# Performance work log

Measured on AMD Instinct MI355X. Metric: run time of the kernel, lower is better.

Reference implementation:

```python
import jax, jax.numpy as jnp
import numpy as np

D_MODEL = 1024
BATCH, HEADS, SEQ, D_HEAD = 4, 16, 2048, D_MODEL // 16


def setup_inputs() -> dict:
    key = jax.random.key(0)
    k1, k2, k3, k4 = jax.random.split(key, 4)
    B = jax.random.normal(k1, (BATCH, HEADS, SEQ, SEQ), dtype=jnp.float32)
    v = jax.random.normal(k2, (BATCH, HEADS, SEQ, D_HEAD), dtype=jnp.float32)
    W = jax.random.normal(k3, (D_MODEL, D_MODEL), dtype=jnp.float32) * (1.0 / np.sqrt(D_MODEL))
    b = jax.random.normal(k4, (D_MODEL,), dtype=jnp.float32) * 0.01
    return {"B": B, "v": v, "W": W, "b": b}


def reference(B, v, W, b):
    # softmax over last (key) axis of the synthesized logits
    p = jax.nn.softmax(B, axis=-1)                      # [b, h, s, s]
    attn = jnp.einsum("bhqk,bhkd->bhqd", p, v)          # [b, h, s, d_head]
    # permute(0,2,3,1): [b, s, d_head, h], then flatten to [b, s, d_model]
    attn = jnp.transpose(attn, (0, 2, 3, 1))
    attn = attn.reshape(attn.shape[0], attn.shape[1], -1)
    # nn.Linear: x @ W.T + b
    return attn @ W.T + b
```

## Files before the change

### kernel.cpp

```cpp
#include <hip/hip_runtime.h>
#include <hip/hip_bf16.h>
#include <stdint.h>


typedef __attribute__((ext_vector_type(8))) short short8;
typedef __attribute__((ext_vector_type(4))) float float4v;

#define SEQL 2048
#define DH   64
#define NH   16
#define DM   1024

static __device__ inline unsigned short f2bf(float x) {
    unsigned u = __float_as_uint(x);
    unsigned r = (u + 0x7FFFu + ((u >> 16) & 1u)) >> 16;
    return (unsigned short)r;
}

__global__ __launch_bounds__(256) void wperm_kernel(const float* __restrict__ W,
                                                    unsigned short* __restrict__ Wp) {
    int tid = blockIdx.x * 256 + threadIdx.x;
    int j   = tid >> 10;
    int rem = tid & 1023;
    int h   = rem >> 6;
    int d   = rem & 63;
    Wp[tid] = f2bf(W[j * 1024 + d * 16 + h]);
}

__global__ __launch_bounds__(256) void attn_kernel(const float* __restrict__ B,
                                                   const float* __restrict__ V,
                                                   unsigned short* __restrict__ attn_out) {
    __shared__ __align__(16) unsigned short Pb[64 * 72];
    __shared__ __align__(16) unsigned short Vt[64 * 72];
    __shared__ float den[64];

    const int t     = threadIdx.x;
    const int lane  = t & 63;
    const int wv    = t >> 6;
    const int c     = lane & 15;
    const int quad  = lane >> 4;
    const int qtile = blockIdx.x;
    const int bh    = blockIdx.y;

    const long long Bbase = (long long)bh * SEQL * SEQL + (long long)(qtile * 64) * SEQL;
    const int Vbase = bh * (SEQL * DH);

    const int sq  = t >> 2;
    const int skb = (t & 3) * 16;
    const int vd  = t & 63;
    const int vko = (t >> 6) * 16;

    if ((t & 3) == 0) den[sq] = 0.0f;

    float4v acc[4];
#pragma unroll
    for (int i = 0; i < 4; i++) acc[i] = (float4v){0.f, 0.f, 0.f, 0.f};

    for (int kk = 0; kk < SEQL / 64; ++kk) {
        {
            const float* src = B + Bbase + (long long)sq * SEQL + (kk * 64 + skb);
            float xv[16];
            *(float4*)&xv[0]  = ((const float4*)src)[0];
            *(float4*)&xv[4]  = ((const float4*)src)[1];
            *(float4*)&xv[8]  = ((const float4*)src)[2];
            *(float4*)&xv[12] = ((const float4*)src)[3];
            alignas(16) unsigned short pk[16];
            float s = 0.0f;
#pragma unroll
            for (int j = 0; j < 16; j++) {
                float e = __expf(xv[j]);
                s += e;
                pk[j] = f2bf(e);
            }
            *(uint4*)&Pb[sq * 72 + skb]     = *(uint4*)&pk[0];
            *(uint4*)&Pb[sq * 72 + skb + 8] = *(uint4*)&pk[8];
            s += __shfl_xor(s, 1);
            s += __shfl_xor(s, 2);
            if ((t & 3) == 0) den[sq] += s;
        }
        {
            const float* vsrc = V + Vbase + (kk * 64 + vko) * DH + vd;
            alignas(16) unsigned short vp[16];
#pragma unroll
            for (int j = 0; j < 16; j++) vp[j] = f2bf(vsrc[j * DH]);
            *(uint4*)&Vt[vd * 72 + vko]     = *(uint4*)&vp[0];
            *(uint4*)&Vt[vd * 72 + vko + 8] = *(uint4*)&vp[8];
        }
        __syncthreads();
#pragma unroll
        for (int ks = 0; ks < 2; ks++) {
            short8 a = *(const short8*)&Pb[(wv * 16 + c) * 72 + ks * 32 + quad * 8];
#pragma unroll
            for (int nb = 0; nb < 4; nb++) {
                short8 bf = *(const short8*)&Vt[(nb * 16 + c) * 72 + ks * 32 + quad * 8];
                acc[nb] = __builtin_amdgcn_mfma_f32_16x16x32_bf16(a, bf, acc[nb], 0, 0, 0);
            }
        }
        __syncthreads();
    }

#pragma unroll
    for (int rr = 0; rr < 4; rr++) {
        int ql  = wv * 16 + quad * 4 + rr;
        float inv = 1.0f / den[ql];
        int qg  = qtile * 64 + ql;
        unsigned short* dst = attn_out + bh * (SEQL * DH) + qg * DH;
#pragma unroll
        for (int nb = 0; nb < 4; nb++) {
            int d = nb * 16 + c;
            dst[d] = f2bf(acc[nb][rr] * inv);
        }
    }
}

__global__ __launch_bounds__(256) void gemm_kernel(const unsigned short* __restrict__ X,
                                                   const unsigned short* __restrict__ Wp,
                                                   const float* __restrict__ bias,
                                                   float* __restrict__ out) {
    __shared__ __align__(16) unsigned short As[128 * 72];
    __shared__ __align__(16) unsigned short Bs[128 * 72];

    const int t    = threadIdx.x;
    const int lane = t & 63;
    const int wv   = t >> 6;
    const int wm   = wv & 1;
    const int wn   = wv >> 1;
    const int c    = lane & 15;
    const int quad = lane >> 4;

    const int rbase = blockIdx.x * 128;
    const int cbase = blockIdx.y * 128;
    const int b     = rbase >> 11;
    const int q0    = rbase & 2047;

    const int srow = t >> 1;
    const int sseg = (t & 1) * 32;

    float4v acc[4][4];
#pragma unroll
    for (int i = 0; i < 4; i++)
#pragma unroll
        for (int j = 0; j < 4; j++) acc[i][j] = (float4v){0.f, 0.f, 0.f, 0.f};

    for (int kt = 0; kt < 16; ++kt) {
        const unsigned short* asrc = X + (((b * 16 + kt) * 2048 + q0 + srow) * 64 + sseg);
        const unsigned short* bsrc = Wp + ((cbase + srow) * 1024 + kt * 64 + sseg);
        uint4 a0 = ((const uint4*)asrc)[0];
        uint4 a1 = ((const uint4*)asrc)[1];
        uint4 a2 = ((const uint4*)asrc)[2];
        uint4 a3 = ((const uint4*)asrc)[3];
        uint4 b0 = ((const uint4*)bsrc)[0];
        uint4 b1 = ((const uint4*)bsrc)[1];
        uint4 b2 = ((const uint4*)bsrc)[2];
        uint4 b3 = ((const uint4*)bsrc)[3];
        *(uint4*)&As[srow * 72 + sseg]      = a0;
        *(uint4*)&As[srow * 72 + sseg + 8]  = a1;
        *(uint4*)&As[srow * 72 + sseg + 16] = a2;
        *(uint4*)&As[srow * 72 + sseg + 24] = a3;
        *(uint4*)&Bs[srow * 72 + sseg]      = b0;
        *(uint4*)&Bs[srow * 72 + sseg + 8]  = b1;
        *(uint4*)&Bs[srow * 72 + sseg + 16] = b2;
        *(uint4*)&Bs[srow * 72 + sseg + 24] = b3;
        __syncthreads();
#pragma unroll
        for (int ks = 0; ks < 2; ks++) {
            short8 af[4], bfr[4];
#pragma unroll
            for (int i = 0; i < 4; i++)
                af[i] = *(const short8*)&As[(wm * 64 + i * 16 + c) * 72 + ks * 32 + quad * 8];
#pragma unroll
            for (int j = 0; j < 4; j++)
                bfr[j] = *(const short8*)&Bs[(wn * 64 + j * 16 + c) * 72 + ks * 32 + quad * 8];
#pragma unroll
            for (int i = 0; i < 4; i++)
#pragma unroll
                for (int j = 0; j < 4; j++)
                    acc[i][j] = __builtin_amdgcn_mfma_f32_16x16x32_bf16(af[i], bfr[j], acc[i][j], 0, 0, 0);
        }
        __syncthreads();
    }

#pragma unroll
    for (int i = 0; i < 4; i++) {
#pragma unroll
        for (int rr = 0; rr < 4; rr++) {
            int row = rbase + wm * 64 + i * 16 + quad * 4 + rr;
            float* orow = out + (long long)row * 1024 + cbase + wn * 64;
            const float* brow = bias + cbase + wn * 64;
#pragma unroll
            for (int j = 0; j < 4; j++) {
                int col = j * 16 + c;
                orow[col] = acc[i][j][rr] + brow[col];
            }
        }
    }
}

extern "C" void kernel_launch(void* const* d_in, const int* in_sizes, int n_in,
                              void* d_out, int out_size, void* d_ws, size_t ws_size,
                              hipStream_t stream) {
    const float* B    = (const float*)d_in[0];
    const float* V    = (const float*)d_in[1];
    const float* W    = (const float*)d_in[2];
    const float* bias = (const float*)d_in[3];
    float* out        = (float*)d_out;

    unsigned short* attn = (unsigned short*)d_ws;
    unsigned short* Wp   = attn + 4 * NH * SEQL * DH;

    wperm_kernel<<<dim3(4096), dim3(256), 0, stream>>>(W, Wp);
    attn_kernel<<<dim3(32, 64), dim3(256), 0, stream>>>(B, V, attn);
    gemm_kernel<<<dim3(64, 8), dim3(256), 0, stream>>>(attn, Wp, bias, out);
}
```

Baseline: 1.423 ms.

## Pre-transpose V to bf16 and stream softmax logits directly into MFMA registers

Adds a kernel that converts V to bf16 and transposes it into a [bh, d, seq] workspace. The attention kernel then has each wave load its B-logit fragments and Vt fragments straight from global memory into MFMA operand registers. This removes the shared-memory staging, both __syncthreads per tile, and the strided per-element V loads. Exp and packing use the hardware v_cvt_pk_bf16_f32 instruction, and the row sum is reduced with shuffles. The cost is an extra launch and an extra pass over V, and each block re-reads Vt from global/L2 instead of sharing it through LDS.

After: 1.537 ms. +8.0%, slower.

```diff
diff --git a/kernel.cpp b/kernel.cpp
--- a/kernel.cpp
+++ b/kernel.cpp
@@ -1,5 +1,4 @@
 #include <hip/hip_runtime.h>
-#include <hip/hip_bf16.h>
 #include <stdint.h>
 
 
@@ -27,88 +26,99 @@
     Wp[tid] = f2bf(W[j * 1024 + d * 16 + h]);
 }
 
-__global__ __launch_bounds__(256) void attn_kernel(const float* __restrict__ B,
-                                                   const float* __restrict__ V,
-                                                   unsigned short* __restrict__ attn_out) {
-    __shared__ __align__(16) unsigned short Pb[64 * 72];
-    __shared__ __align__(16) unsigned short Vt[64 * 72];
-    __shared__ float den[64];
-
-    const int t     = threadIdx.x;
-    const int lane  = t & 63;
-    const int wv    = t >> 6;
-    const int c     = lane & 15;
-    const int quad  = lane >> 4;
-    const int qtile = blockIdx.x;
-    const int bh    = blockIdx.y;
-
-    const long long Bbase = (long long)bh * SEQL * SEQL + (long long)(qtile * 64) * SEQL;
-    const int Vbase = bh * (SEQL * DH);
-
-    const int sq  = t >> 2;
-    const int skb = (t & 3) * 16;
-    const int vd  = t & 63;
-    const int vko = (t >> 6) * 16;
-
-    if ((t & 3) == 0) den[sq] = 0.0f;
+__global__ __launch_bounds__(256) void vtperm_kernel(const float* __restrict__ V,
+                                                     unsigned short* __restrict__ Vt) {
+    __shared__ __align__(16) unsigned short T[64 * 72];
+    const int t  = threadIdx.x;
+    const int bh = blockIdx.y;
+    const int k0 = blockIdx.x * 64;
+    {
+        const int kl = t >> 2;
+        const int d0 = (t & 3) * 16;
+        const float* src = V + ((long long)(bh * SEQL + k0 + kl)) * DH + d0;
+        float x[16];
+        *(float4*)&x[0]  = ((const float4*)src)[0];
+        *(float4*)&x[4]  = ((const float4*)src)[1];
+        *(float4*)&x[8]  = ((const float4*)src)[2];
+        *(float4*)&x[12] = ((const float4*)src)[3];
+#pragma unroll
+        for (int j = 0; j < 16; j++) T[(d0 + j) * 72 + kl] = f2bf(x[j]);
+    }
+    __syncthreads();
+    {
+        const int dd = t >> 2;
+        const int ks = (t & 3) * 16;
+        unsigned short* dst = Vt + ((long long)(bh * DH + dd)) * SEQL + k0 + ks;
+        *(uint4*)dst       = *(uint4*)&T[dd * 72 + ks];
+        *(uint4*)(dst + 8) = *(uint4*)&T[dd * 72 + ks + 8];
+    }
+}
+
+__global__ __launch_bounds__(256, 2) void attn_kernel(const float* __restrict__ B,
+                                                      const unsigned short* __restrict__ Vt,
+                                                      unsigned short* __restrict__ attn_out) {
+    const int t    = threadIdx.x;
+    const int lane = t & 63;
+    const int wv   = t >> 6;
+    const int c    = lane & 15;
+    const int quad = lane >> 4;
+    const int qt   = blockIdx.x;
+    const int bh   = blockIdx.y;
+    const int q0   = qt * 64 + wv * 16;
+
+    const float* Brow = B + ((long long)(bh * SEQL + q0 + c)) * SEQL + quad * 8;
+    const unsigned short* Vb = Vt + ((long long)(bh * DH + c)) * SEQL + quad * 8;
 
     float4v acc[4];
 #pragma unroll
     for (int i = 0; i < 4; i++) acc[i] = (float4v){0.f, 0.f, 0.f, 0.f};
-
-    for (int kk = 0; kk < SEQL / 64; ++kk) {
-        {
-            const float* src = B + Bbase + (long long)sq * SEQL + (kk * 64 + skb);
-            float xv[16];
-            *(float4*)&xv[0]  = ((const float4*)src)[0];
-            *(float4*)&xv[4]  = ((const float4*)src)[1];
-            *(float4*)&xv[8]  = ((const float4*)src)[2];
-            *(float4*)&xv[12] = ((const float4*)src)[3];
-            alignas(16) unsigned short pk[16];
-            float s = 0.0f;
-#pragma unroll
-            for (int j = 0; j < 16; j++) {
-                float e = __expf(xv[j]);
-                s += e;
-                pk[j] = f2bf(e);
-            }
-            *(uint4*)&Pb[sq * 72 + skb]     = *(uint4*)&pk[0];
-            *(uint4*)&Pb[sq * 72 + skb + 8] = *(uint4*)&pk[8];
-            s += __shfl_xor(s, 1);
-            s += __shfl_xor(s, 2);
-            if ((t & 3) == 0) den[sq] += s;
-        }
-        {
-            const float* vsrc = V + Vbase + (kk * 64 + vko) * DH + vd;
-            alignas(16) unsigned short vp[16];
-#pragma unroll
-            for (int j = 0; j < 16; j++) vp[j] = f2bf(vsrc[j * DH]);
-            *(uint4*)&Vt[vd * 72 + vko]     = *(uint4*)&vp[0];
-            *(uint4*)&Vt[vd * 72 + vko + 8] = *(uint4*)&vp[8];
-        }
-        __syncthreads();
-#pragma unroll
-        for (int ks = 0; ks < 2; ks++) {
-            short8 a = *(const short8*)&Pb[(wv * 16 + c) * 72 + ks * 32 + quad * 8];
-#pragma unroll
-            for (int nb = 0; nb < 4; nb++) {
-                short8 bf = *(const short8*)&Vt[(nb * 16 + c) * 72 + ks * 32 + quad * 8];
-                acc[nb] = __builtin_amdgcn_mfma_f32_16x16x32_bf16(a, bf, acc[nb], 0, 0, 0);
-            }
-        }
-        __syncthreads();
-    }
-
+    float den = 0.f;
+
+    for (int kk = 0; kk < SEQL; kk += 64) {
+        float x[16];
+        *(float4*)&x[0]  = *(const float4*)(Brow + kk);
+        *(float4*)&x[4]  = *(const float4*)(Brow + kk + 4);
+        *(float4*)&x[8]  = *(const float4*)(Brow + kk + 32);
+        *(float4*)&x[12] = *(const float4*)(Brow + kk + 36);
+
+        short8 bfr0[4], bfr1[4];
+#pragma unroll
+        for (int nb = 0; nb < 4; nb++) {
+            bfr0[nb] = *(const short8*)(Vb + nb * 16 * SEQL + kk);
+            bfr1[nb] = *(const short8*)(Vb + nb * 16 * SEQL + kk + 32);
+        }
+
+        float s = 0.f;
+#pragma unroll
+        for (int j = 0; j < 16; j++) { x[j] = __expf(x[j]); s += x[j]; }
+        den += s;
+
+        union { unsigned int u[8]; short8 v[2]; } A;
+#pragma unroll
+        for (int j = 0; j < 8; j++) {
+            unsigned int r;
+            asm("v_cvt_pk_bf16_f32 %0, %1, %2" : "=v"(r) : "v"(x[2 * j]), "v"(x[2 * j + 1]));
+            A.u[j] = r;
+        }
+
+#pragma unroll
+        for (int nb = 0; nb < 4; nb++) {
+            acc[nb] = __builtin_amdgcn_mfma_f32_16x16x32_bf16(A.v[0], bfr0[nb], acc[nb], 0, 0, 0);
+            acc[nb] = __builtin_amdgcn_mfma_f32_16x16x32_bf16(A.v[1], bfr1[nb], acc[nb], 0, 0, 0);
+        }
+    }
+
+    den += __shfl_xor(den, 16);
+    den += __shfl_xor(den, 32);
+
+    unsigned short* dst0 = attn_out + ((long long)(bh * SEQL + q0)) * DH;
 #pragma unroll
     for (int rr = 0; rr < 4; rr++) {
-        int ql  = wv * 16 + quad * 4 + rr;
-        float inv = 1.0f / den[ql];
-        int qg  = qtile * 64 + ql;
-        unsigned short* dst = attn_out + bh * (SEQL * DH) + qg * DH;
+        const int ql = quad * 4 + rr;
+        const float inv = 1.0f / __shfl(den, ql);
 #pragma unroll
         for (int nb = 0; nb < 4; nb++) {
-            int d = nb * 16 + c;
-            dst[d] = f2bf(acc[nb][rr] * inv);
+            dst0[ql * DH + nb * 16 + c] = f2bf(acc[nb][rr] * inv);
         }
     }
 }
@@ -207,8 +217,10 @@
 
     unsigned short* attn = (unsigned short*)d_ws;
     unsigned short* Wp   = attn + 4 * NH * SEQL * DH;
+    unsigned short* Vt   = Wp + DM * DM;
 
     wperm_kernel<<<dim3(4096), dim3(256), 0, stream>>>(W, Wp);
-    attn_kernel<<<dim3(32, 64), dim3(256), 0, stream>>>(B, V, attn);
+    vtperm_kernel<<<dim3(32, 64), dim3(256), 0, stream>>>(V, Vt);
+    attn_kernel<<<dim3(32, 64), dim3(256), 0, stream>>>(B, Vt, attn);
     gemm_kernel<<<dim3(64, 8), dim3(256), 0, stream>>>(attn, Wp, bias, out);
 }
```
